# Kernel tuning notes

Measured on AMD Instinct MI355X. Metric: run time of the kernel, lower is better.

Reference implementation:

```python
import jax, jax.numpy as jnp
import numpy as np
import math

B, T, C, H = 4, 1024, 1024, 16
R = 32.0
MAX_SPAN = 1024  # block_size
SPAN_REG = 2e-06


def setup_inputs() -> dict:
    key = jax.random.key(0)
    k1, k2, k3 = jax.random.split(key, 3)
    x = jax.random.normal(k1, (B, T, C), dtype=jnp.float32)
    Wqkv = jax.random.normal(k2, (C, 3 * C), dtype=jnp.float32) * 0.02
    Wproj = jax.random.normal(k3, (C, C), dtype=jnp.float32) * 0.02
    span_params = jnp.zeros((H,), dtype=jnp.float32)
    stride_params = jnp.zeros((H, 2), dtype=jnp.float32)
    return {"x": x, "Wqkv": Wqkv, "Wproj": Wproj,
            "span_params": span_params, "stride_params": stride_params}


def reference(x, Wqkv, Wproj, span_params, stride_params):
    b, t, c = x.shape
    h = span_params.shape[0]
    hd = c // h

    qkv = x @ Wqkv                                  # [B,T,3C]
    q, k, v = jnp.split(qkv, 3, axis=-1)
    q = q.reshape(b, t, h, hd).transpose(0, 2, 1, 3)  # [B,H,T,hd]
    k = k.reshape(b, t, h, hd).transpose(0, 2, 1, 3)
    v = v.reshape(b, t, h, hd).transpose(0, 2, 1, 3)

    att = jnp.einsum('bhqd,bhkd->bhqk', q, k) * (1.0 / math.sqrt(hd))

    i = jnp.arange(t)[:, None]
    j = jnp.arange(t)[None, :]
    rel = (i - j).astype(jnp.float32)               # relative position i-j
    causal = i >= j                                 # stride-1 pattern == tril
    allowed2 = (i == j) | ((i > j) & ((i - j) % 2 == 0))  # stride-2 pattern

    spans = jax.nn.sigmoid(span_params) * MAX_SPAN  # [H]
    sw = jax.nn.softmax(stride_params, axis=-1)     # [H,2]

    sp = spans[:, None, None]                       # [H,1,1]
    # soft ramp mask: 1 inside span, linear falloff over R, 0 outside / disallowed
    m1 = jnp.where(causal,  jnp.clip((R + sp - rel) / R, 0.0, 1.0), 0.0)  # [H,T,T]
    m2 = jnp.where(allowed2, jnp.clip((R + sp - rel) / R, 0.0, 1.0), 0.0)
    mask = sw[:, 0, None, None] * m1 + sw[:, 1, None, None] * m2          # [H,T,T]

    # unnormalized exp weighting (no max-subtraction), causal -inf fill
    wexp = jnp.exp(jnp.where(causal, att, -jnp.inf)) * mask               # [B,H,T,T]
    att_n = wexp / jnp.sum(wexp, axis=-1, keepdims=True)

    y = jnp.einsum('bhqk,bhkd->bhqd', att_n, v)
    y = y.transpose(0, 2, 1, 3).reshape(b, t, c)
    y = y @ Wproj

    span_loss = SPAN_REG * jnp.sum(spans) / h
    return y, span_loss
```

## Files before the change

kernel.cpp:

```cpp
#include <hip/hip_runtime.h>
#include <math.h>

#define BATCH 4
#define SEQ   1024
#define CH    1024
#define NH    16
#define HD    64
#define N3    3072

typedef unsigned short u16;
typedef unsigned int   u32;
typedef __attribute__((ext_vector_type(8))) __bf16 bf16x8;
typedef __attribute__((ext_vector_type(4))) float  f32x4;
typedef __attribute__((ext_vector_type(4))) u32    u32x4;

__device__ __forceinline__ u32 f2bf(float f) {
    u32 x = __float_as_uint(f);
    return (x + 0x7fffu + ((x >> 16) & 1u)) >> 16;
}

__global__ __launch_bounds__(256) void conv_bf16_kernel(
    const float* __restrict__ in, u16* __restrict__ out, int n)
{
    int i = (blockIdx.x * 256 + threadIdx.x) * 8;
    if (i >= n) return;
    float4 a = *(const float4*)&in[i];
    float4 b = *(const float4*)&in[i + 4];
    int4 p;
    p.x = (int)(f2bf(a.x) | (f2bf(a.y) << 16));
    p.y = (int)(f2bf(a.z) | (f2bf(a.w) << 16));
    p.z = (int)(f2bf(b.x) | (f2bf(b.y) << 16));
    p.w = (int)(f2bf(b.z) | (f2bf(b.w) << 16));
    *(int4*)&out[i] = p;
}

__global__ __launch_bounds__(256) void transpose_conv_kernel(
    const float* __restrict__ W, u16* __restrict__ WT, int K, int N)
{
    __shared__ float tile[32][33];
    const int n0 = blockIdx.x * 32, k0 = blockIdx.y * 32;
    const int tx = threadIdx.x & 31, ty = threadIdx.x >> 5;
    #pragma unroll
    for (int p = 0; p < 4; p++)
        tile[ty + p * 8][tx] = W[(size_t)(k0 + ty + p * 8) * N + n0 + tx];
    __syncthreads();
    #pragma unroll
    for (int p = 0; p < 4; p++)
        WT[(size_t)(n0 + ty + p * 8) * K + k0 + tx] = (u16)f2bf(tile[tx][ty + p * 8]);
}

__global__ __launch_bounds__(256) void gemm_qkv_mfma(
    const u16* __restrict__ A, const u16* __restrict__ BT,
    u16* __restrict__ qb, u16* __restrict__ kbuf, u16* __restrict__ vbuf)
{
    __shared__ __align__(16) u16 As[128 * 32];
    __shared__ __align__(16) u16 Bs[128 * 32];

    const int tid = threadIdx.x;
    const int lane = tid & 63;
    const int w = tid >> 6;
    const int wr = w >> 1, wc = w & 1;
    const int m0 = blockIdx.y * 128, n0 = blockIdx.x * 128;

    const int sr = tid >> 2;
    const int sc = (tid & 3) * 8;
    const u16* Ag0 = A  + (size_t)(m0 + sr) * CH + sc;
    const u16* Ag1 = A  + (size_t)(m0 + 64 + sr) * CH + sc;
    const u16* Bg0 = BT + (size_t)(n0 + sr) * CH + sc;
    const u16* Bg1 = BT + (size_t)(n0 + 64 + sr) * CH + sc;

    const int ln = lane & 15, quad = lane >> 4;
    const int afo = (wr * 64 + ln) * 32 + quad * 8;
    const int bfo = (wc * 64 + ln) * 32 + quad * 8;

    f32x4 acc[4][4];
    #pragma unroll
    for (int i = 0; i < 4; i++)
        #pragma unroll
        for (int j = 0; j < 4; j++) acc[i][j] = (f32x4)(0.f);

    for (int k0 = 0; k0 < CH; k0 += 32) {
        int4 a0 = *(const int4*)(Ag0 + k0);
        int4 a1 = *(const int4*)(Ag1 + k0);
        int4 b0 = *(const int4*)(Bg0 + k0);
        int4 b1 = *(const int4*)(Bg1 + k0);
        __syncthreads();
        *(int4*)&As[sr * 32 + sc]        = a0;
        *(int4*)&As[(sr + 64) * 32 + sc] = a1;
        *(int4*)&Bs[sr * 32 + sc]        = b0;
        *(int4*)&Bs[(sr + 64) * 32 + sc] = b1;
        __syncthreads();
        bf16x8 af[4], bfr[4];
        #pragma unroll
        for (int mi = 0; mi < 4; mi++) af[mi]  = *(const bf16x8*)&As[afo + mi * 512];
        #pragma unroll
        for (int ni = 0; ni < 4; ni++) bfr[ni] = *(const bf16x8*)&Bs[bfo + ni * 512];
        #pragma unroll
        for (int mi = 0; mi < 4; mi++)
            #pragma unroll
            for (int ni = 0; ni < 4; ni++)
                acc[mi][ni] = __builtin_amdgcn_mfma_f32_16x16x32_bf16(
                    af[mi], bfr[ni], acc[mi][ni], 0, 0, 0);
    }

    #pragma unroll
    for (int ni = 0; ni < 4; ni++) {
        const int n = n0 + wc * 64 + ni * 16 + ln;
        const int which = n >> 10;
        const int h = (n >> 6) & 15;
        const int d = n & 63;
        u16* dst = (which == 0) ? qb : (which == 1) ? kbuf : vbuf;
        #pragma unroll
        for (int mi = 0; mi < 4; mi++) {
            #pragma unroll
            for (int r = 0; r < 4; r++) {
                const int m = m0 + wr * 64 + mi * 16 + quad * 4 + r;
                const int b = m >> 10, t = m & 1023;
                dst[(((size_t)(b * NH + h)) * SEQ + t) * HD + d] =
                    (u16)f2bf(acc[mi][ni][r]);
            }
        }
    }
}

__global__ __launch_bounds__(256) void gemm_proj_mfma(
    const u16* __restrict__ A, const u16* __restrict__ BT, float* __restrict__ out)
{
    __shared__ __align__(16) u16 As[128 * 32];
    __shared__ __align__(16) u16 Bs[128 * 32];

    const int tid = threadIdx.x;
    const int lane = tid & 63;
    const int w = tid >> 6;
    const int wr = w >> 1, wc = w & 1;
    const int m0 = blockIdx.y * 128, n0 = blockIdx.x * 128;

    const int sr = tid >> 2;
    const int sc = (tid & 3) * 8;
    const u16* Ag0 = A  + (size_t)(m0 + sr) * CH + sc;
    const u16* Ag1 = A  + (size_t)(m0 + 64 + sr) * CH + sc;
    const u16* Bg0 = BT + (size_t)(n0 + sr) * CH + sc;
    const u16* Bg1 = BT + (size_t)(n0 + 64 + sr) * CH + sc;

    const int ln = lane & 15, quad = lane >> 4;
    const int afo = (wr * 64 + ln) * 32 + quad * 8;
    const int bfo = (wc * 64 + ln) * 32 + quad * 8;

    f32x4 acc[4][4];
    #pragma unroll
    for (int i = 0; i < 4; i++)
        #pragma unroll
        for (int j = 0; j < 4; j++) acc[i][j] = (f32x4)(0.f);

    for (int k0 = 0; k0 < CH; k0 += 32) {
        int4 a0 = *(const int4*)(Ag0 + k0);
        int4 a1 = *(const int4*)(Ag1 + k0);
        int4 b0 = *(const int4*)(Bg0 + k0);
        int4 b1 = *(const int4*)(Bg1 + k0);
        __syncthreads();
        *(int4*)&As[sr * 32 + sc]        = a0;
        *(int4*)&As[(sr + 64) * 32 + sc] = a1;
        *(int4*)&Bs[sr * 32 + sc]        = b0;
        *(int4*)&Bs[(sr + 64) * 32 + sc] = b1;
        __syncthreads();
        bf16x8 af[4], bfr[4];
        #pragma unroll
        for (int mi = 0; mi < 4; mi++) af[mi]  = *(const bf16x8*)&As[afo + mi * 512];
        #pragma unroll
        for (int ni = 0; ni < 4; ni++) bfr[ni] = *(const bf16x8*)&Bs[bfo + ni * 512];
        #pragma unroll
        for (int mi = 0; mi < 4; mi++)
            #pragma unroll
            for (int ni = 0; ni < 4; ni++)
                acc[mi][ni] = __builtin_amdgcn_mfma_f32_16x16x32_bf16(
                    af[mi], bfr[ni], acc[mi][ni], 0, 0, 0);
    }

    #pragma unroll
    for (int ni = 0; ni < 4; ni++) {
        const int n = n0 + wc * 64 + ni * 16 + ln;
        #pragma unroll
        for (int mi = 0; mi < 4; mi++) {
            #pragma unroll
            for (int r = 0; r < 4; r++) {
                const int m = m0 + wr * 64 + mi * 16 + quad * 4 + r;
                out[(size_t)m * CH + n] = acc[mi][ni][r];
            }
        }
    }
}

__global__ __launch_bounds__(256) void attn_mfma_kernel(
    const u16* __restrict__ qg, const u16* __restrict__ kg,
    const u16* __restrict__ vg,
    const float* __restrict__ span_params, const float* __restrict__ stride_params,
    u16* __restrict__ yb)
{
    __shared__ float tab[1056];
    __shared__ u32   VTs[64 * 33];
    __shared__ __align__(16) u16 Ps[4 * 16 * 72];

    const int tid  = threadIdx.x;
    const int lane = tid & 63;
    const int w    = tid >> 6;
    const int ln   = lane & 15, quad = lane >> 4;

    const int blk = blockIdx.x;
    const int it  = blk & 15;
    const int bh  = blk >> 4;
    const int h   = bh & (NH - 1);
    const int b   = bh >> 4;
    const int it0 = it << 6;
    const int row_base = it0 + (w << 4);

    const float span  = 1024.f / (1.f + __expf(-span_params[h]));
    const float limit = 32.f + span;
    const float e0 = __expf(stride_params[2 * h + 0]);
    const float e1 = __expf(stride_params[2 * h + 1]);
    const float inv_e = 1.f / (e0 + e1);
    const float sw0 = e0 * inv_e, sw1 = e1 * inv_e;

    for (int i = tid; i < 1056; i += 256) {
        int rel = i - 32;
        float clipv = fminf(fmaxf((limit - (float)rel) * (1.f / 32.f), 0.f), 1.f);
        float mw = (rel < 0) ? 0.f : clipv * (sw0 + ((rel & 1) ? 0.f : sw1));
        tab[i] = mw;
    }

    const size_t hb = (size_t)bh * SEQ;

    const u16* qp = qg + (hb + row_base + ln) * HD + quad * 8;
    bf16x8 aq0 = *(const bf16x8*)qp;
    bf16x8 aq1 = *(const bf16x8*)(qp + 32);

    u32x4 onesw; onesw.x = onesw.y = onesw.z = onesw.w = 0x3f803f80u;
    const bf16x8 onesf = __builtin_bit_cast(bf16x8, onesw);

    f32x4 acc_o[4];
    #pragma unroll
    for (int di = 0; di < 4; di++) acc_o[di] = (f32x4)(0.f);
    f32x4 acc_s = (f32x4)(0.f);

    int jmin = it0 - (int)limit - 1;
    if (jmin < 0) jmin = 0;
    const int jt0 = jmin & ~63;

    const int dc = tid & 7, jp = tid >> 3;

    u16* Psw = &Ps[w * 16 * 72];

    __syncthreads();

    for (int jt = jt0; jt <= it0; jt += 64) {
        const u16* vp = vg + (hb + jt + 2 * jp) * HD + dc * 8;
        int4 v0 = *(const int4*)vp;
        int4 v1 = *(const int4*)(vp + HD);
        __syncthreads();
        {
            u32 a, bb;
            a = (u32)v0.x; bb = (u32)v1.x;
            VTs[(8 * dc + 0) * 33 + jp] = (a & 0xffffu) | (bb << 16);
            VTs[(8 * dc + 1) * 33 + jp] = (a >> 16) | (bb & 0xffff0000u);
            a = (u32)v0.y; bb = (u32)v1.y;
            VTs[(8 * dc + 2) * 33 + jp] = (a & 0xffffu) | (bb << 16);
            VTs[(8 * dc + 3) * 33 + jp] = (a >> 16) | (bb & 0xffff0000u);
            a = (u32)v0.z; bb = (u32)v1.z;
            VTs[(8 * dc + 4) * 33 + jp] = (a & 0xffffu) | (bb << 16);
            VTs[(8 * dc + 5) * 33 + jp] = (a >> 16) | (bb & 0xffff0000u);
            a = (u32)v0.w; bb = (u32)v1.w;
            VTs[(8 * dc + 6) * 33 + jp] = (a & 0xffffu) | (bb << 16);
            VTs[(8 * dc + 7) * 33 + jp] = (a >> 16) | (bb & 0xffff0000u);
        }

        #pragma unroll
        for (int ni = 0; ni < 4; ni++) {
            const int col0 = jt + ni * 16;
            const int rel_max = row_base + 15 - col0;
            const int rel_min = row_base - (col0 + 15);
            if (rel_max < 0 || (float)rel_min >= limit) {
                #pragma unroll
                for (int r = 0; r < 4; r++)
                    Psw[(quad * 4 + r) * 72 + ni * 16 + ln] = 0;
                continue;
            }
            const u16* kp = kg + (hb + col0 + ln) * HD + quad * 8;
            bf16x8 bk0 = *(const bf16x8*)kp;
            bf16x8 bk1 = *(const bf16x8*)(kp + 32);
            f32x4 s = __builtin_amdgcn_mfma_f32_16x16x32_bf16(aq0, bk0, (f32x4)(0.f), 0, 0, 0);
            s = __builtin_amdgcn_mfma_f32_16x16x32_bf16(aq1, bk1, s, 0, 0, 0);
            #pragma unroll
            for (int r = 0; r < 4; r++) {
                const int rel = (row_base + quad * 4 + r) - (col0 + ln);
                float wv = __expf(s[r] * 0.125f) * tab[rel + 32];
                Psw[(quad * 4 + r) * 72 + ni * 16 + ln] = (u16)f2bf(wv);
            }
        }

        __syncthreads();

        bf16x8 ap0 = *(const bf16x8*)&Psw[ln * 72 + quad * 8];
        bf16x8 ap1 = *(const bf16x8*)&Psw[ln * 72 + 32 + quad * 8];
        acc_s = __builtin_amdgcn_mfma_f32_16x16x32_bf16(ap0, onesf, acc_s, 0, 0, 0);
        acc_s = __builtin_amdgcn_mfma_f32_16x16x32_bf16(ap1, onesf, acc_s, 0, 0, 0);
        #pragma unroll
        for (int di = 0; di < 4; di++) {
            const int base0 = (di * 16 + ln) * 33 + quad * 4;
            u32x4 c0, c1;
            c0.x = VTs[base0 + 0]; c0.y = VTs[base0 + 1];
            c0.z = VTs[base0 + 2]; c0.w = VTs[base0 + 3];
            c1.x = VTs[base0 + 16]; c1.y = VTs[base0 + 17];
            c1.z = VTs[base0 + 18]; c1.w = VTs[base0 + 19];
            bf16x8 bv0 = __builtin_bit_cast(bf16x8, c0);
            bf16x8 bv1 = __builtin_bit_cast(bf16x8, c1);
            acc_o[di] = __builtin_amdgcn_mfma_f32_16x16x32_bf16(ap0, bv0, acc_o[di], 0, 0, 0);
            acc_o[di] = __builtin_amdgcn_mfma_f32_16x16x32_bf16(ap1, bv1, acc_o[di], 0, 0, 0);
        }
    }

    #pragma unroll
    for (int r = 0; r < 4; r++) {
        const int t = row_base + quad * 4 + r;
        const float inv = 1.f / acc_s[r];
        const size_t rowoff = ((size_t)(b * SEQ + t)) * CH + h * HD;
        #pragma unroll
        for (int di = 0; di < 4; di++)
            yb[rowoff + di * 16 + ln] = (u16)f2bf(acc_o[di][r] * inv);
    }
}

__global__ void span_loss_kernel(const float* __restrict__ sp, float* __restrict__ out)
{
    if (threadIdx.x == 0 && blockIdx.x == 0) {
        float s = 0.f;
        for (int h = 0; h < NH; h++) {
            float sig = 1.f / (1.f + __expf(-sp[h]));
            s += sig * 1024.f;
        }
        out[0] = 2e-6f * s / (float)NH;
    }
}

extern "C" void kernel_launch(void* const* d_in, const int* in_sizes, int n_in,
                              void* d_out, int out_size, void* d_ws, size_t ws_size,
                              hipStream_t stream)
{
    const float* x            = (const float*)d_in[0];
    const float* Wqkv         = (const float*)d_in[1];
    const float* Wproj        = (const float*)d_in[2];
    const float* span_params  = (const float*)d_in[3];
    const float* stride_param = (const float*)d_in[4];
    float* out = (float*)d_out;

    const size_t SZ = (size_t)BATCH * NH * SEQ * HD;
    u16* base = (u16*)d_ws;
    u16* qb  = base;
    u16* kb  = qb + SZ;
    u16* vb  = kb + SZ;
    u16* yb  = vb + SZ;
    u16* xb  = yb + SZ;
    u16* wqT = xb + SZ;
    u16* wpT = wqT + (size_t)CH * N3;

    conv_bf16_kernel<<<dim3((int)(SZ / (256 * 8))), 256, 0, stream>>>(x, xb, (int)SZ);
    transpose_conv_kernel<<<dim3(N3 / 32, CH / 32), 256, 0, stream>>>(Wqkv, wqT, CH, N3);
    transpose_conv_kernel<<<dim3(CH / 32, CH / 32), 256, 0, stream>>>(Wproj, wpT, CH, CH);

    gemm_qkv_mfma<<<dim3(N3 / 128, (BATCH * SEQ) / 128), 256, 0, stream>>>(
        xb, wqT, qb, kb, vb);

    attn_mfma_kernel<<<dim3(BATCH * NH * (SEQ / 64)), 256, 0, stream>>>(
        qb, kb, vb, span_params, stride_param, yb);

    gemm_proj_mfma<<<dim3(CH / 128, (BATCH * SEQ) / 128), 256, 0, stream>>>(
        yb, wpT, out);

    span_loss_kernel<<<1, 64, 0, stream>>>(span_params, out + SZ);
}
```

Baseline: 194.6 us.

## Use direct global-to-LDS loads in GEMMs, pre-transpose V, restructure attention loop

The QKV and projection GEMMs now stage tiles with global_load_lds, which writes global data straight into shared memory instead of going through registers. The projection GEMM uses 64-row M tiles so more blocks are launched. A new kernel pre-transposes V, so attention loads K and V fragments directly from global memory, drops the in-loop LDS V transpose and a block barrier, and uses an XOR-swizzled per-wave P buffer. Fully masked 32-column halves now skip their MFMAs. The cost is an extra kernel launch, a second V buffer in the workspace, and the loss of the barrier that previously separated P writes from P reads.

```diff
diff --git a/kernel.cpp b/kernel.cpp
--- a/kernel.cpp
+++ b/kernel.cpp
@@ -17,6 +17,12 @@
 __device__ __forceinline__ u32 f2bf(float f) {
     u32 x = __float_as_uint(f);
     return (x + 0x7fffu + ((x >> 16) & 1u)) >> 16;
+}
+
+__device__ __forceinline__ void gload_lds16(const u16* g, u16* l) {
+    __builtin_amdgcn_global_load_lds(
+        (const __attribute__((address_space(1))) void*)g,
+        (__attribute__((address_space(3))) void*)l, 16, 0, 0);
 }
 
 __global__ __launch_bounds__(256) void conv_bf16_kernel(
@@ -49,6 +55,27 @@
         WT[(size_t)(n0 + ty + p * 8) * K + k0 + tx] = (u16)f2bf(tile[tx][ty + p * 8]);
 }
 
+__global__ __launch_bounds__(256) void transpose_v_kernel(
+    const u16* __restrict__ v, u16* __restrict__ vt)
+{
+    __shared__ u16 tile[64][72];
+    const int bh = blockIdx.x >> 4, tt = blockIdx.x & 15;
+    const int t0 = tt * 64;
+    const int r = threadIdx.x >> 2, c = (threadIdx.x & 3) * 16;
+    const u16* src = v + ((size_t)bh * SEQ + t0) * HD;
+    *(int4*)&tile[r][c]     = *(const int4*)&src[(size_t)r * HD + c];
+    *(int4*)&tile[r][c + 8] = *(const int4*)&src[(size_t)r * HD + c + 8];
+    __syncthreads();
+    const int d = r, c2 = c;
+    u32 buf[8];
+    #pragma unroll
+    for (int q = 0; q < 8; q++)
+        buf[q] = (u32)tile[c2 + 2 * q][d] | ((u32)tile[c2 + 2 * q + 1][d] << 16);
+    u16* dst = vt + ((size_t)bh * HD + d) * SEQ + t0 + c2;
+    *(int4*)dst       = make_int4((int)buf[0], (int)buf[1], (int)buf[2], (int)buf[3]);
+    *(int4*)(dst + 8) = make_int4((int)buf[4], (int)buf[5], (int)buf[6], (int)buf[7]);
+}
+
 __global__ __launch_bounds__(256) void gemm_qkv_mfma(
     const u16* __restrict__ A, const u16* __restrict__ BT,
     u16* __restrict__ qb, u16* __restrict__ kbuf, u16* __restrict__ vbuf)
@@ -62,12 +89,16 @@
     const int wr = w >> 1, wc = w & 1;
     const int m0 = blockIdx.y * 128, n0 = blockIdx.x * 128;
 
-    const int sr = tid >> 2;
-    const int sc = (tid & 3) * 8;
-    const u16* Ag0 = A  + (size_t)(m0 + sr) * CH + sc;
-    const u16* Ag1 = A  + (size_t)(m0 + 64 + sr) * CH + sc;
-    const u16* Bg0 = BT + (size_t)(n0 + sr) * CH + sc;
-    const u16* Bg1 = BT + (size_t)(n0 + 64 + sr) * CH + sc;
+    const int srow = lane >> 2;
+    const int sk   = (lane & 3) * 8;
+    const u16* gA0 = A  + (size_t)(m0 + w * 16 + srow) * CH + sk;
+    const u16* gA1 = A  + (size_t)(m0 + (w + 4) * 16 + srow) * CH + sk;
+    const u16* gB0 = BT + (size_t)(n0 + w * 16 + srow) * CH + sk;
+    const u16* gB1 = BT + (size_t)(n0 + (w + 4) * 16 + srow) * CH + sk;
+    u16* lA0 = As + w * 16 * 32;
+    u16* lA1 = As + (w + 4) * 16 * 32;
+    u16* lB0 = Bs + w * 16 * 32;
+    u16* lB1 = Bs + (w + 4) * 16 * 32;
 
     const int ln = lane & 15, quad = lane >> 4;
     const int afo = (wr * 64 + ln) * 32 + quad * 8;
@@ -80,15 +111,11 @@
         for (int j = 0; j < 4; j++) acc[i][j] = (f32x4)(0.f);
 
     for (int k0 = 0; k0 < CH; k0 += 32) {
-        int4 a0 = *(const int4*)(Ag0 + k0);
-        int4 a1 = *(const int4*)(Ag1 + k0);
-        int4 b0 = *(const int4*)(Bg0 + k0);
-        int4 b1 = *(const int4*)(Bg1 + k0);
         __syncthreads();
-        *(int4*)&As[sr * 32 + sc]        = a0;
-        *(int4*)&As[(sr + 64) * 32 + sc] = a1;
-        *(int4*)&Bs[sr * 32 + sc]        = b0;
-        *(int4*)&Bs[(sr + 64) * 32 + sc] = b1;
+        gload_lds16(gA0 + k0, lA0);
+        gload_lds16(gA1 + k0, lA1);
+        gload_lds16(gB0 + k0, lB0);
+        gload_lds16(gB1 + k0, lB1);
         __syncthreads();
         bf16x8 af[4], bfr[4];
         #pragma unroll
@@ -126,50 +153,47 @@
 __global__ __launch_bounds__(256) void gemm_proj_mfma(
     const u16* __restrict__ A, const u16* __restrict__ BT, float* __restrict__ out)
 {
-    __shared__ __align__(16) u16 As[128 * 32];
+    __shared__ __align__(16) u16 As[64 * 32];
     __shared__ __align__(16) u16 Bs[128 * 32];
 
     const int tid = threadIdx.x;
     const int lane = tid & 63;
     const int w = tid >> 6;
     const int wr = w >> 1, wc = w & 1;
-    const int m0 = blockIdx.y * 128, n0 = blockIdx.x * 128;
-
-    const int sr = tid >> 2;
-    const int sc = (tid & 3) * 8;
-    const u16* Ag0 = A  + (size_t)(m0 + sr) * CH + sc;
-    const u16* Ag1 = A  + (size_t)(m0 + 64 + sr) * CH + sc;
-    const u16* Bg0 = BT + (size_t)(n0 + sr) * CH + sc;
-    const u16* Bg1 = BT + (size_t)(n0 + 64 + sr) * CH + sc;
+    const int m0 = blockIdx.y * 64, n0 = blockIdx.x * 128;
+
+    const int srow = lane >> 2;
+    const int sk   = (lane & 3) * 8;
+    const u16* gA0 = A  + (size_t)(m0 + w * 16 + srow) * CH + sk;
+    const u16* gB0 = BT + (size_t)(n0 + w * 16 + srow) * CH + sk;
+    const u16* gB1 = BT + (size_t)(n0 + (w + 4) * 16 + srow) * CH + sk;
+    u16* lA0 = As + w * 16 * 32;
+    u16* lB0 = Bs + w * 16 * 32;
+    u16* lB1 = Bs + (w + 4) * 16 * 32;
 
     const int ln = lane & 15, quad = lane >> 4;
-    const int afo = (wr * 64 + ln) * 32 + quad * 8;
+    const int afo = (wr * 32 + ln) * 32 + quad * 8;
     const int bfo = (wc * 64 + ln) * 32 + quad * 8;
 
-    f32x4 acc[4][4];
-    #pragma unroll
-    for (int i = 0; i < 4; i++)
+    f32x4 acc[2][4];
+    #pragma unroll
+    for (int i = 0; i < 2; i++)
         #pragma unroll
         for (int j = 0; j < 4; j++) acc[i][j] = (f32x4)(0.f);
 
     for (int k0 = 0; k0 < CH; k0 += 32) {
-        int4 a0 = *(const int4*)(Ag0 + k0);
-        int4 a1 = *(const int4*)(Ag1 + k0);
-        int4 b0 = *(const int4*)(Bg0 + k0);
-        int4 b1 = *(const int4*)(Bg1 + k0);
         __syncthreads();
-        *(int4*)&As[sr * 32 + sc]        = a0;
-        *(int4*)&As[(sr + 64) * 32 + sc] = a1;
-        *(int4*)&Bs[sr * 32 + sc]        = b0;
-        *(int4*)&Bs[(sr + 64) * 32 + sc] = b1;
+        gload_lds16(gA0 + k0, lA0);
+        gload_lds16(gB0 + k0, lB0);
+        gload_lds16(gB1 + k0, lB1);
         __syncthreads();
-        bf16x8 af[4], bfr[4];
-        #pragma unroll
-        for (int mi = 0; mi < 4; mi++) af[mi]  = *(const bf16x8*)&As[afo + mi * 512];
+        bf16x8 af[2], bfr[4];
+        #pragma unroll
+        for (int mi = 0; mi < 2; mi++) af[mi]  = *(const bf16x8*)&As[afo + mi * 512];
         #pragma unroll
         for (int ni = 0; ni < 4; ni++) bfr[ni] = *(const bf16x8*)&Bs[bfo + ni * 512];
         #pragma unroll
-        for (int mi = 0; mi < 4; mi++)
+        for (int mi = 0; mi < 2; mi++)
             #pragma unroll
             for (int ni = 0; ni < 4; ni++)
                 acc[mi][ni] = __builtin_amdgcn_mfma_f32_16x16x32_bf16(
@@ -180,10 +204,10 @@
     for (int ni = 0; ni < 4; ni++) {
         const int n = n0 + wc * 64 + ni * 16 + ln;
         #pragma unroll
-        for (int mi = 0; mi < 4; mi++) {
+        for (int mi = 0; mi < 2; mi++) {
             #pragma unroll
             for (int r = 0; r < 4; r++) {
-                const int m = m0 + wr * 64 + mi * 16 + quad * 4 + r;
+                const int m = m0 + wr * 32 + mi * 16 + quad * 4 + r;
                 out[(size_t)m * CH + n] = acc[mi][ni][r];
             }
         }
@@ -192,13 +216,12 @@
 
 __global__ __launch_bounds__(256) void attn_mfma_kernel(
     const u16* __restrict__ qg, const u16* __restrict__ kg,
-    const u16* __restrict__ vg,
+    const u16* __restrict__ vt,
     const float* __restrict__ span_params, const float* __restrict__ stride_params,
     u16* __restrict__ yb)
 {
     __shared__ float tab[1056];
-    __shared__ u32   VTs[64 * 33];
-    __shared__ __align__(16) u16 Ps[4 * 16 * 72];
+    __shared__ __align__(16) u16 Ps[4][16 * 64];
 
     const int tid  = threadIdx.x;
     const int lane = tid & 63;
@@ -223,11 +246,11 @@
     for (int i = tid; i < 1056; i += 256) {
         int rel = i - 32;
         float clipv = fminf(fmaxf((limit - (float)rel) * (1.f / 32.f), 0.f), 1.f);
-        float mw = (rel < 0) ? 0.f : clipv * (sw0 + ((rel & 1) ? 0.f : sw1));
-        tab[i] = mw;
-    }
-
-    const size_t hb = (size_t)bh * SEQ;
+        tab[i] = (rel < 0) ? 0.f : clipv * (sw0 + ((rel & 1) ? 0.f : sw1));
+    }
+
+    const size_t hb  = (size_t)bh * SEQ;
+    const size_t hvt = (size_t)bh * HD;
 
     const u16* qp = qg + (hb + row_base + ln) * HD + quad * 8;
     bf16x8 aq0 = *(const bf16x8*)qp;
@@ -245,75 +268,74 @@
     if (jmin < 0) jmin = 0;
     const int jt0 = jmin & ~63;
 
-    const int dc = tid & 7, jp = tid >> 3;
-
-    u16* Psw = &Ps[w * 16 * 72];
+    u16* Psw = Ps[w];
+    const int lm7 = ln & 7;
 
     __syncthreads();
 
     for (int jt = jt0; jt <= it0; jt += 64) {
-        const u16* vp = vg + (hb + jt + 2 * jp) * HD + dc * 8;
-        int4 v0 = *(const int4*)vp;
-        int4 v1 = *(const int4*)(vp + HD);
-        __syncthreads();
-        {
-            u32 a, bb;
-            a = (u32)v0.x; bb = (u32)v1.x;
-            VTs[(8 * dc + 0) * 33 + jp] = (a & 0xffffu) | (bb << 16);
-            VTs[(8 * dc + 1) * 33 + jp] = (a >> 16) | (bb & 0xffff0000u);
-            a = (u32)v0.y; bb = (u32)v1.y;
-            VTs[(8 * dc + 2) * 33 + jp] = (a & 0xffffu) | (bb << 16);
-            VTs[(8 * dc + 3) * 33 + jp] = (a >> 16) | (bb & 0xffff0000u);
-            a = (u32)v0.z; bb = (u32)v1.z;
-            VTs[(8 * dc + 4) * 33 + jp] = (a & 0xffffu) | (bb << 16);
-            VTs[(8 * dc + 5) * 33 + jp] = (a >> 16) | (bb & 0xffff0000u);
-            a = (u32)v0.w; bb = (u32)v1.w;
-            VTs[(8 * dc + 6) * 33 + jp] = (a & 0xffffu) | (bb << 16);
-            VTs[(8 * dc + 7) * 33 + jp] = (a >> 16) | (bb & 0xffff0000u);
-        }
-
+        bf16x8 kf[4][2], vf[4][2];
+        #pragma unroll
+        for (int ni = 0; ni < 4; ni++) {
+            const u16* kp = kg + (hb + jt + ni * 16 + ln) * HD + quad * 8;
+            kf[ni][0] = *(const bf16x8*)kp;
+            kf[ni][1] = *(const bf16x8*)(kp + 32);
+        }
+        #pragma unroll
+        for (int di = 0; di < 4; di++) {
+            const u16* vp = vt + (hvt + di * 16 + ln) * SEQ + jt + quad * 8;
+            vf[di][0] = *(const bf16x8*)vp;
+            vf[di][1] = *(const bf16x8*)(vp + 32);
+        }
+
+        bool sk[4];
         #pragma unroll
         for (int ni = 0; ni < 4; ni++) {
             const int col0 = jt + ni * 16;
-            const int rel_max = row_base + 15 - col0;
-            const int rel_min = row_base - (col0 + 15);
-            if (rel_max < 0 || (float)rel_min >= limit) {
-                #pragma unroll
-                for (int r = 0; r < 4; r++)
-                    Psw[(quad * 4 + r) * 72 + ni * 16 + ln] = 0;
+            sk[ni] = (row_base + 15 < col0) ||
+                     ((float)(row_base - (col0 + 15)) >= limit);
+        }
+        const bool nz0 = !sk[0] || !sk[1];
+        const bool nz1 = !sk[2] || !sk[3];
+
+        #pragma unroll
+        for (int ni = 0; ni < 4; ni++) {
+            const int col0 = jt + ni * 16;
+            const int cbase = ni * 2 + (ln >> 3);
+            if (sk[ni]) {
+                if ((ni < 2) ? nz0 : nz1) {
+                    #pragma unroll
+                    for (int r = 0; r < 4; r++) {
+                        const int il = quad * 4 + r;
+                        Psw[il * 64 + (cbase ^ (il & 7)) * 8 + lm7] = 0;
+                    }
+                }
                 continue;
             }
-            const u16* kp = kg + (hb + col0 + ln) * HD + quad * 8;
-            bf16x8 bk0 = *(const bf16x8*)kp;
-            bf16x8 bk1 = *(const bf16x8*)(kp + 32);
-            f32x4 s = __builtin_amdgcn_mfma_f32_16x16x32_bf16(aq0, bk0, (f32x4)(0.f), 0, 0, 0);
-            s = __builtin_amdgcn_mfma_f32_16x16x32_bf16(aq1, bk1, s, 0, 0, 0);
+            f32x4 s = __builtin_amdgcn_mfma_f32_16x16x32_bf16(aq0, kf[ni][0], (f32x4)(0.f), 0, 0, 0);
+            s = __builtin_amdgcn_mfma_f32_16x16x32_bf16(aq1, kf[ni][1], s, 0, 0, 0);
             #pragma unroll
             for (int r = 0; r < 4; r++) {
-                const int rel = (row_base + quad * 4 + r) - (col0 + ln);
+                const int il  = quad * 4 + r;
+                const int rel = (row_base + il) - (col0 + ln);
                 float wv = __expf(s[r] * 0.125f) * tab[rel + 32];
-                Psw[(quad * 4 + r) * 72 + ni * 16 + ln] = (u16)f2bf(wv);
+                Psw[il * 64 + (cbase ^ (il & 7)) * 8 + lm7] = (u16)f2bf(wv);
             }
         }
 
-        __syncthreads();
-
-        bf16x8 ap0 = *(const bf16x8*)&Psw[ln * 72 + quad * 8];
-        bf16x8 ap1 = *(const bf16x8*)&Psw[ln * 72 + 32 + quad * 8];
-        acc_s = __builtin_amdgcn_mfma_f32_16x16x32_bf16(ap0, onesf, acc_s, 0, 0, 0);
-        acc_s = __builtin_amdgcn_mfma_f32_16x16x32_bf16(ap1, onesf, acc_s, 0, 0, 0);
-        #pragma unroll
-        for (int di = 0; di < 4; di++) {
-            const int base0 = (di * 16 + ln) * 33 + quad * 4;
-            u32x4 c0, c1;
-            c0.x = VTs[base0 + 0]; c0.y = VTs[base0 + 1];
-            c0.z = VTs[base0 + 2]; c0.w = VTs[base0 + 3];
-            c1.x = VTs[base0 + 16]; c1.y = VTs[base0 + 17];
-            c1.z = VTs[base0 + 18]; c1.w = VTs[base0 + 19];
-            bf16x8 bv0 = __builtin_bit_cast(bf16x8, c0);
-            bf16x8 bv1 = __builtin_bit_cast(bf16x8, c1);
-            acc_o[di] = __builtin_amdgcn_mfma_f32_16x16x32_bf16(ap0, bv0, acc_o[di], 0, 0, 0);
-            acc_o[di] = __builtin_amdgcn_mfma_f32_16x16x32_bf16(ap1, bv1, acc_o[di], 0, 0, 0);
+        if (nz0) {
+            bf16x8 ap0 = *(const bf16x8*)&Psw[ln * 64 + (quad ^ lm7) * 8];
+            acc_s = __builtin_amdgcn_mfma_f32_16x16x32_bf16(ap0, onesf, acc_s, 0, 0, 0);
+            #pragma unroll
+            for (int di = 0; di < 4; di++)
+                acc_o[di] = __builtin_amdgcn_mfma_f32_16x16x32_bf16(ap0, vf[di][0], acc_o[di], 0, 0, 0);
+        }
+        if (nz1) {
+            bf16x8 ap1 = *(const bf16x8*)&Psw[ln * 64 + ((quad + 4) ^ lm7) * 8];
+            acc_s = __builtin_amdgcn_mfma_f32_16x16x32_bf16(ap1, onesf, acc_s, 0, 0, 0);
+            #pragma unroll
+            for (int di = 0; di < 4; di++)
+                acc_o[di] = __builtin_amdgcn_mfma_f32_16x16x32_bf16(ap1, vf[di][1], acc_o[di], 0, 0, 0);
         }
     }
 
@@ -356,7 +378,8 @@
     u16* qb  = base;
     u16* kb  = qb + SZ;
     u16* vb  = kb + SZ;
-    u16* yb  = vb + SZ;
+    u16* vtb = vb + SZ;
+    u16* yb  = vtb + SZ;
     u16* xb  = yb + SZ;
     u16* wqT = xb + SZ;
     u16* wpT = wqT + (size_t)CH * N3;
@@ -368,10 +391,12 @@
     gemm_qkv_mfma<<<dim3(N3 / 128, (BATCH * SEQ) / 128), 256, 0, stream>>>(
         xb, wqT, qb, kb, vb);
 
+    transpose_v_kernel<<<dim3(BATCH * NH * (SEQ / 64)), 256, 0, stream>>>(vb, vtb);
+
     attn_mfma_kernel<<<dim3(BATCH * NH * (SEQ / 64)), 256, 0, stream>>>(
-        qb, kb, vb, span_params, stride_param, yb);
-
-    gemm_proj_mfma<<<dim3(CH / 128, (BATCH * SEQ) / 128), 256, 0, stream>>>(
+        qb, kb, vtb, span_params, stride_param, yb);
+
+    gemm_proj_mfma<<<dim3(CH / 128, (BATCH * SEQ) / 64), 256, 0, stream>>>(
         yb, wpT, out);
 
     span_loss_kernel<<<1, 64, 0, stream>>>(span_params, out + SZ);
```

Result: slower. 228.8 us (+17.6%).
